# Kernel optimization log

Measured on AMD Instinct MI355X. Metric: run time of the kernel, lower is better.

The kernel has to match this reference:

```python
import jax, jax.numpy as jnp
import numpy as np

B, N, D, H = 4, 2048, 512, 8
DH = D // H
EPS = 1e-6


def setup_inputs() -> dict:
    key = jax.random.key(0)
    ks = jax.random.split(key, 12)
    s = 1.0 / np.sqrt(D)
    return {
        "x": jax.random.normal(ks[0], (B, N, D), jnp.float32),
        "attn_bias": jax.random.normal(ks[1], (B, 1, N, N), jnp.float32),
        "Wq": jax.random.normal(ks[2], (D, D), jnp.float32) * s,
        "bq": jnp.zeros((D,), jnp.float32),
        "Wk": jax.random.normal(ks[3], (D, D), jnp.float32) * s,
        "bk": jnp.zeros((D,), jnp.float32),
        "Wv": jax.random.normal(ks[4], (D, D), jnp.float32) * s,
        "bv": jnp.zeros((D,), jnp.float32),
        "Wo": jax.random.normal(ks[5], (D, D), jnp.float32) * s,
        "bo": jnp.zeros((D,), jnp.float32),
        "q_gamma": jnp.ones((DH,), jnp.float32),
        "q_beta": jnp.zeros((DH,), jnp.float32),
        "k_gamma": jnp.ones((DH,), jnp.float32),
        "k_beta": jnp.zeros((DH,), jnp.float32),
    }


def _layernorm(x, gamma, beta):
    mu = jnp.mean(x, axis=-1, keepdims=True)
    var = jnp.var(x, axis=-1, keepdims=True)
    return (x - mu) * jax.lax.rsqrt(var + EPS) * gamma + beta


def reference(x, attn_bias, Wq, bq, Wk, bk, Wv, bv, Wo, bo,
              q_gamma, q_beta, k_gamma, k_beta):
    b, n, d = x.shape
    # project and split heads: (B, H, N, DH)
    def heads(W, bias):
        return (x @ W.T + bias).reshape(b, n, H, DH).transpose(0, 2, 1, 3)
    q = heads(Wq, bq)
    k = heads(Wk, bk)
    v = heads(Wv, bv)
    q = _layernorm(q, q_gamma, q_beta)
    k = _layernorm(k, k_gamma, k_beta)
    scores = jnp.einsum('bhqd,bhkd->bhqk', q, k) / np.sqrt(DH)
    scores = scores + attn_bias  # (B,1,N,N) broadcasts over heads
    attn = jax.nn.softmax(scores, axis=-1)
    out = jnp.einsum('bhqk,bhkd->bhqd', attn, v)
    out = out.transpose(0, 2, 1, 3).reshape(b, n, d)
    return out @ Wo.T + bo
```

## Files before the change

kernel.cpp:

```cpp
#include <hip/hip_runtime.h>

typedef __attribute__((ext_vector_type(8))) short short8;
typedef __attribute__((ext_vector_type(4))) float f32x4;
typedef __attribute__((ext_vector_type(4))) int i32x4;
typedef __attribute__((ext_vector_type(4))) unsigned short u16x4;
typedef __attribute__((ext_vector_type(8))) unsigned short u16x8;
typedef __attribute__((ext_vector_type(2))) unsigned int u32x2;

#define B_  4
#define N_  2048
#define D_  512
#define H_  8
#define DH_ 64
#define M_  (B_ * N_)

__device__ __forceinline__ unsigned short f2bf(float f) {
    union { float f; unsigned u; } un; un.f = f;
    unsigned r = un.u + 0x7FFFu + ((un.u >> 16) & 1u);
    return (unsigned short)(r >> 16);
}
__device__ __forceinline__ float exp2fast(float x) {
#if __has_builtin(__builtin_amdgcn_exp2f)
    return __builtin_amdgcn_exp2f(x);
#else
    float r; asm("v_exp_f32 %0, %1" : "=v"(r) : "v"(x)); return r;
#endif
}
__device__ __forceinline__ unsigned cvtpk_bf16(float lo, float hi) {
    unsigned r;
    asm("v_cvt_pk_bf16_f32 %0, %1, %2" : "=v"(r) : "v"(lo), "v"(hi));
    return r;
}
__device__ __forceinline__ float max3f(float a, float b, float c) {
    return fmaxf(fmaxf(a, b), c);
}

typedef __attribute__((address_space(1))) const void gvoid;
typedef __attribute__((address_space(3))) void svoid;
__device__ __forceinline__ void load16_lds(const void* g, void* s) {
    __builtin_amdgcn_global_load_lds((gvoid*)g, (svoid*)s, 16, 0, 0);
}

__global__ __launch_bounds__(256) void cvt_all(
    const float* __restrict__ x,
    const float* __restrict__ W0, const float* __restrict__ W1,
    const float* __restrict__ W2, const float* __restrict__ W3,
    unsigned short* __restrict__ xb, unsigned short* __restrict__ Wb) {
    const int bx = blockIdx.x;
    const float* src;
    unsigned short* dst;
    int i;
    if (bx < 4096) {
        src = x; dst = xb;
        i = (bx * 256 + (int)threadIdx.x) * 4;
    } else {
        const int r = bx - 4096;
        const int sel = r >> 8;
        src = (sel == 0) ? W0 : (sel == 1) ? W1 : (sel == 2) ? W2 : W3;
        dst = Wb + (size_t)sel * D_ * D_;
        i = ((r & 255) * 256 + (int)threadIdx.x) * 4;
    }
    f32x4 v = *(const f32x4*)(src + i);
    u16x4 o;
    o[0] = f2bf(v[0]); o[1] = f2bf(v[1]); o[2] = f2bf(v[2]); o[3] = f2bf(v[3]);
    *(u16x4*)(dst + i) = o;
}

template <bool F32OUT, bool LNF>
__global__ __launch_bounds__(256, 2) void gemm_nt(
    const unsigned short* __restrict__ A,
    const unsigned short* __restrict__ W,
    const float* __restrict__ Bv0,
    const float* __restrict__ Bv1,
    const float* __restrict__ Bv2,
    const float* __restrict__ g0, const float* __restrict__ be0,
    const float* __restrict__ g1, const float* __restrict__ be1,
    unsigned short* __restrict__ outb,
    float* __restrict__ outf)
{
    const int mt = blockIdx.x;
    const int nt = blockIdx.y;
    const int sel = nt >> 2;
    const unsigned short* Wp = W + (size_t)sel * D_ * D_;
    const float* Bv = (sel == 0) ? Bv0 : (sel == 1) ? Bv1 : Bv2;
    const int n0 = (nt & 3) * 128;

    __shared__ __align__(16) unsigned short As[128 * 32];
    __shared__ __align__(16) unsigned short Bs[128 * 32];

    const int tid = threadIdx.x;
    const int w   = tid >> 6;
    const int l   = tid & 63;
    const int l15 = l & 15;
    const int qd  = l >> 4;
    const int wr  = w >> 1;
    const int wc  = w & 1;

    int srow[2], scol[2];
#pragma unroll
    for (int c = 0; c < 2; ++c) {
        const int g   = (w * 2 + c) * 64 + l;
        const int row = g >> 2;
        srow[c] = row;
        scol[c] = ((g & 3) ^ (row & 3)) * 8;
    }

    f32x4 acc[4][4];
#pragma unroll
    for (int i = 0; i < 4; ++i)
#pragma unroll
        for (int j = 0; j < 4; ++j)
            acc[i][j] = (f32x4){0.f, 0.f, 0.f, 0.f};

    const int swz = qd ^ (l15 & 3);

    for (int k0 = 0; k0 < D_; k0 += 32) {
        __syncthreads();
#pragma unroll
        for (int c = 0; c < 2; ++c) {
            load16_lds(A  + (size_t)(mt * 128 + srow[c]) * D_ + k0 + scol[c],
                       As + (w * 2 + c) * 512);
            load16_lds(Wp + (size_t)(n0 + srow[c]) * D_ + k0 + scol[c],
                       Bs + (w * 2 + c) * 512);
        }
        __syncthreads();

        short8 af[4], bfr[4];
#pragma unroll
        for (int rt = 0; rt < 4; ++rt)
            af[rt] = *(const short8*)&As[(wr * 64 + rt * 16 + l15) * 32 + swz * 8];
#pragma unroll
        for (int ct = 0; ct < 4; ++ct)
            bfr[ct] = *(const short8*)&Bs[(wc * 64 + ct * 16 + l15) * 32 + swz * 8];
#pragma unroll
        for (int rt = 0; rt < 4; ++rt)
#pragma unroll
            for (int ct = 0; ct < 4; ++ct)
                acc[rt][ct] = __builtin_amdgcn_mfma_f32_16x16x32_bf16(
                    af[rt], bfr[ct], acc[rt][ct], 0, 0, 0);
    }

    const float* gam = (sel == 0) ? g0 : g1;
    const float* bet = (sel == 0) ? be0 : be1;
    float gv[4], bv2[4];
    if (LNF) {
#pragma unroll
        for (int ct = 0; ct < 4; ++ct) { gv[ct] = gam[ct * 16 + l15]; bv2[ct] = bet[ct * 16 + l15]; }
    }

#pragma unroll
    for (int rt = 0; rt < 4; ++rt) {
        float v[4][4];
#pragma unroll
        for (int ct = 0; ct < 4; ++ct) {
            const float bias = Bv[n0 + wc * 64 + ct * 16 + l15];
#pragma unroll
            for (int r = 0; r < 4; ++r) v[ct][r] = acc[rt][ct][r] + bias;
        }
        if (LNF && sel < 2) {
#pragma unroll
            for (int r = 0; r < 4; ++r) {
                float s  = v[0][r] + v[1][r] + v[2][r] + v[3][r];
                float s2 = v[0][r]*v[0][r] + v[1][r]*v[1][r] + v[2][r]*v[2][r] + v[3][r]*v[3][r];
#pragma unroll
                for (int o = 1; o <= 8; o <<= 1) {
                    s  += __shfl_xor(s, o);
                    s2 += __shfl_xor(s2, o);
                }
                const float mu  = s * 0.015625f;
                const float var = s2 * 0.015625f - mu * mu;
                const float rs  = rsqrtf(var + 1e-6f);
#pragma unroll
                for (int ct = 0; ct < 4; ++ct)
                    v[ct][r] = (v[ct][r] - mu) * rs * gv[ct] + bv2[ct];
            }
        }
#pragma unroll
        for (int ct = 0; ct < 4; ++ct) {
            const int col  = n0 + wc * 64 + ct * 16 + l15;
            const int row0 = mt * 128 + wr * 64 + rt * 16 + qd * 4;
#pragma unroll
            for (int r = 0; r < 4; ++r) {
                const size_t oidx = (size_t)(row0 + r) * D_ + col;
                if (F32OUT) outf[oidx] = v[ct][r];
                else        outb[(size_t)sel * M_ * D_ + oidx] = f2bf(v[ct][r]);
            }
        }
    }
}

__global__ __launch_bounds__(256) void pack_kv(
    const unsigned short* __restrict__ K, const unsigned short* __restrict__ V,
    unsigned short* __restrict__ Kt, unsigned short* __restrict__ Vt2)
{
    const int nt = blockIdx.x, b = blockIdx.y;
    const int tid = threadIdx.x;
    __shared__ __align__(16) unsigned short Vl[64][520];

#pragma unroll
    for (int i = 0; i < 16; ++i) {
        const int c = i * 256 + tid;
        const int row = c >> 6, ch = c & 63;
        const size_t srow = ((size_t)(b * N_ + nt * 64 + row)) * D_ + ch * 8;
        i32x4 kd = *(const i32x4*)(K + srow);
        const int h = ch >> 3, dc = ch & 7;
        *(i32x4*)(Kt + ((((size_t)(b * 8 + h) * 32 + nt) * 64 + row) * 64) + dc * 8) = kd;
        i32x4 vd = *(const i32x4*)(V + srow);
        *(i32x4*)&Vl[row][ch * 8] = vd;
    }
    __syncthreads();
#pragma unroll
    for (int i = 0; i < 16; ++i) {
        const int c = i * 256 + tid;
        const int h = c >> 9, r = c & 511;
        const int dh = r >> 3, kc = r & 7;
        u16x4 o0, o1;
#pragma unroll
        for (int j = 0; j < 4; ++j) o0[j] = Vl[kc * 8 + j][h * 64 + dh];
#pragma unroll
        for (int j = 0; j < 4; ++j) o1[j] = Vl[kc * 8 + 4 + j][h * 64 + dh];
        const int t = kc >> 1;
        const int col0 = (t & 2) * 16 + (kc & 1) * 16 + (t & 1) * 4;
        const size_t rowbase = ((((size_t)(b * 8 + h) * 32 + nt) * 64 + dh) * 64);
        *(u16x4*)(Vt2 + rowbase + col0)     = o0;
        *(u16x4*)(Vt2 + rowbase + col0 + 8) = o1;
    }
}

__global__ __launch_bounds__(512, 4) void attn12(
    const unsigned short* __restrict__ Qm,
    const unsigned short* __restrict__ Kt,
    const unsigned short* __restrict__ Vt2,
    const float* __restrict__ Bias,
    unsigned short* __restrict__ AO)
{
    const int qt = blockIdx.x;
    const int h  = blockIdx.y;
    const int b  = blockIdx.z;
    const int w  = threadIdx.x >> 6;
    const int l  = threadIdx.x & 63;
    const int l15 = l & 15;
    const int qd  = l >> 4;
    const int q0 = qt * 128 + w * 16;
    const float L2E = 1.4426950408889634f;

    __shared__ __align__(16) unsigned char smem[32768];

    const int c    = w * 64 + l;
    const int srow = c >> 3;
    const int sg   = (c & 7) ^ (srow & 7);
    const int soff = srow * 64 + sg * 8;
    const int sc16 = c * 16;

    short8 qf[2];
#pragma unroll
    for (int hf = 0; hf < 2; ++hf)
        qf[hf] = *(const short8*)(Qm +
            (size_t)(b * N_ + q0 + l15) * D_ + h * DH_ + hf * 32 + qd * 8);

    f32x4 Ot[4];
#pragma unroll
    for (int rt = 0; rt < 4; ++rt) Ot[rt] = (f32x4){0.f, 0.f, 0.f, 0.f};
    float m_i = -3.0e38f;
    f32x4 li4 = (f32x4){0.f, 0.f, 0.f, 0.f};

    const unsigned short* Ktile0 = Kt  + (((size_t)(b * 8 + h) * 32) * 64) * 64;
    const unsigned short* Vtile0 = Vt2 + (((size_t)(b * 8 + h) * 32) * 64) * 64;
    const float* biasQ = Bias + ((size_t)b * N_ + q0 + l15) * N_;

    load16_lds(Ktile0 + soff, smem + sc16);
    load16_lds(Vtile0 + soff, smem + 8192 + sc16);
    f32x4 brA[4], brB[4];
#pragma unroll
    for (int rt = 0; rt < 4; ++rt)
        brA[rt] = *(const f32x4*)(biasQ + rt * 16 + qd * 4);
    asm volatile("s_waitcnt vmcnt(0)" ::: "memory");

#define ATTN_ITER(KT, CUR, BRC, BRN) do {                                      \
    unsigned char* Kbc = smem + (CUR) * 16384;                                 \
    unsigned char* Vbc = Kbc + 8192;                                           \
    asm volatile("s_waitcnt vmcnt(4)" ::: "memory");                           \
    __builtin_amdgcn_s_barrier();                                              \
    __builtin_amdgcn_sched_barrier(0);                                         \
    if ((KT) < 31) {                                                           \
        const unsigned short* Kn = Ktile0 + (size_t)((KT) + 1) * 4096;         \
        const unsigned short* Vn = Vtile0 + (size_t)((KT) + 1) * 4096;         \
        unsigned char* KbN = smem + (((CUR) ^ 1)) * 16384;                     \
        load16_lds(Kn + soff, KbN + sc16);                                     \
        load16_lds(Vn + soff, KbN + 8192 + sc16);                              \
    }                                                                          \
    asm volatile("" ::: "memory");       \
    {                                                                          \
        const float* Bn = biasQ + (size_t)(((KT) < 31) ? (KT) + 1 : 31) * 64;  \
        _Pragma("unroll")                                                      \
        for (int rt = 0; rt < 4; ++rt)                                         \
            BRN[rt] = *(const f32x4*)(Bn + rt * 16 + qd * 4);                  \
    }                                                                          \
    short8 kf[4][2];                                                           \
    _Pragma("unroll")                                                          \
    for (int rt = 0; rt < 4; ++rt) {                                           \
        const int kv = rt * 16 + l15;                                          \
        _Pragma("unroll")                                                      \
        for (int hf = 0; hf < 2; ++hf) {                                       \
            const int cidx = (hf * 4 + qd) ^ (kv & 7);                         \
            kf[rt][hf] = *(const short8*)(Kbc + kv * 128 + cidx * 16);         \
        }                                                                      \
    }                                                                          \
    f32x4 St[4];                                                               \
    __builtin_amdgcn_s_setprio(1);                                             \
    _Pragma("unroll")                                                          \
    for (int rt = 0; rt < 4; ++rt) {                                           \
        f32x4 v = (f32x4){0.f, 0.f, 0.f, 0.f};                                 \
        v = __builtin_amdgcn_mfma_f32_16x16x32_bf16(kf[rt][0], qf[0], v, 0, 0, 0); \
        v = __builtin_amdgcn_mfma_f32_16x16x32_bf16(kf[rt][1], qf[1], v, 0, 0, 0); \
        St[rt] = v;                                                            \
    }                                                                          \
    __builtin_amdgcn_s_setprio(0);                                             \
    short8 vf[4][2];                                                           \
    _Pragma("unroll")                                                          \
    for (int rt = 0; rt < 4; ++rt) {                                           \
        const int dh = rt * 16 + l15;                                          \
        _Pragma("unroll")                                                      \
        for (int hf = 0; hf < 2; ++hf) {                                       \
            const int cidx = (hf * 4 + qd) ^ (dh & 7);                         \
            vf[rt][hf] = *(const short8*)(Vbc + dh * 128 + cidx * 16);         \
        }                                                                      \
    }                                                                          \
    unsigned wq[4][2];                                                         \
    {                                                                          \
        f32x4 sv[4];                                                           \
        _Pragma("unroll")                                                      \
        for (int rt = 0; rt < 4; ++rt)                                         \
            sv[rt] = St[rt] * 0.125f + BRC[rt];                                \
        float mx0 = max3f(sv[0][0], sv[0][1], sv[0][2]);                       \
        float mx1 = max3f(sv[0][3], sv[1][0], sv[1][1]);                       \
        float mx2 = max3f(sv[1][2], sv[1][3], sv[2][0]);                       \
        float mx3 = max3f(sv[2][1], sv[2][2], sv[2][3]);                       \
        mx0 = max3f(mx0, sv[3][0], sv[3][1]);                                  \
        mx1 = max3f(mx1, sv[3][2], sv[3][3]);                                  \
        float mx = fmaxf(max3f(mx0, mx1, mx2), mx3);                           \
        mx = fmaxf(mx, __shfl_xor(mx, 16));                                    \
        mx = fmaxf(mx, __shfl_xor(mx, 32));                                    \
        if (__any(mx > m_i + 8.0f)) {                                          \
            const float mnew  = fmaxf(m_i, mx);                                \
            const float alpha = exp2fast((m_i - mnew) * L2E);                  \
            m_i = mnew;                                                        \
            li4 *= alpha;                                                      \
            _Pragma("unroll")                                                  \
            for (int rt = 0; rt < 4; ++rt) Ot[rt] *= alpha;                    \
        }                                                                      \
        const float mL = m_i * L2E;                                            \
        f32x4 p[4];                                                            \
        _Pragma("unroll")                                                      \
        for (int rt = 0; rt < 4; ++rt) {                                       \
            f32x4 e = sv[rt] * L2E - mL;                                       \
            p[rt][0] = exp2fast(e[0]); p[rt][1] = exp2fast(e[1]);              \
            p[rt][2] = exp2fast(e[2]); p[rt][3] = exp2fast(e[3]);              \
        }                                                                      \
        li4 += (p[0] + p[1]) + (p[2] + p[3]);                                  \
        _Pragma("unroll")                                                      \
        for (int rt = 0; rt < 4; ++rt) {                                       \
            wq[rt][0] = cvtpk_bf16(p[rt][0], p[rt][1]);                        \
            wq[rt][1] = cvtpk_bf16(p[rt][2], p[rt][3]);                        \
        }                                                                      \
    }                                                                          \
                           \
    union { unsigned u[4]; short8 s; } pk0, pk1;                               \
    pk0.u[0] = wq[0][0]; pk0.u[1] = wq[0][1];                                  \
    pk0.u[2] = wq[1][0]; pk0.u[3] = wq[1][1];                                  \
    pk1.u[0] = wq[2][0]; pk1.u[1] = wq[2][1];                                  \
    pk1.u[2] = wq[3][0]; pk1.u[3] = wq[3][1];                                  \
    __builtin_amdgcn_s_setprio(1);                                             \
    _Pragma("unroll")                                                          \
    for (int rt = 0; rt < 4; ++rt) {                                           \
        Ot[rt] = __builtin_amdgcn_mfma_f32_16x16x32_bf16(vf[rt][0], pk0.s, Ot[rt], 0, 0, 0); \
        Ot[rt] = __builtin_amdgcn_mfma_f32_16x16x32_bf16(vf[rt][1], pk1.s, Ot[rt], 0, 0, 0); \
    }                                                                          \
    __builtin_amdgcn_s_setprio(0);                                             \
} while (0)

    for (int kt2 = 0; kt2 < 16; ++kt2) {
        ATTN_ITER(kt2 * 2,     0, brA, brB);
        ATTN_ITER(kt2 * 2 + 1, 1, brB, brA);
    }
#undef ATTN_ITER

    float l_i = (li4[0] + li4[1]) + (li4[2] + li4[3]);
    l_i += __shfl_xor(l_i, 16);
    l_i += __shfl_xor(l_i, 32);
    const float inv = 1.f / l_i;
    const int q = q0 + l15;
#pragma unroll
    for (int rt = 0; rt < 4; ++rt) {
        u16x4 ob;
#pragma unroll
        for (int r = 0; r < 4; ++r) ob[r] = f2bf(Ot[rt][r] * inv);
        *(u16x4*)(AO + (size_t)(b * N_ + q) * D_ + h * DH_ + rt * 16 + qd * 4) = ob;
    }
}

extern "C" void kernel_launch(void* const* d_in, const int* in_sizes, int n_in,
                              void* d_out, int out_size, void* d_ws, size_t ws_size,
                              hipStream_t stream) {
    const float* x  = (const float*)d_in[0];
    const float* ab = (const float*)d_in[1];
    const float* Wq = (const float*)d_in[2];
    const float* bq = (const float*)d_in[3];
    const float* Wk = (const float*)d_in[4];
    const float* bk = (const float*)d_in[5];
    const float* Wv = (const float*)d_in[6];
    const float* bv = (const float*)d_in[7];
    const float* Wo = (const float*)d_in[8];
    const float* bo = (const float*)d_in[9];
    const float* qg = (const float*)d_in[10];
    const float* qb = (const float*)d_in[11];
    const float* kg = (const float*)d_in[12];
    const float* kb = (const float*)d_in[13];

    unsigned short* xb  = (unsigned short*)d_ws;
    unsigned short* Wb  = xb  + (size_t)M_ * D_;
    unsigned short* Y   = Wb  + (size_t)4 * D_ * D_;
    unsigned short* Kt  = Y   + (size_t)3 * M_ * D_;
    unsigned short* Vt2 = Kt  + (size_t)M_ * D_;
    unsigned short* AO  = Vt2 + (size_t)M_ * D_;
    float* out = (float*)d_out;

    cvt_all<<<dim3(5120), dim3(256), 0, stream>>>(x, Wq, Wk, Wv, Wo, xb, Wb);

    gemm_nt<false, true><<<dim3(64, 12), dim3(256), 0, stream>>>(
        xb, Wb, bq, bk, bv, qg, qb, kg, kb, Y, nullptr);

    pack_kv<<<dim3(32, 4), dim3(256), 0, stream>>>(
        Y + (size_t)M_ * D_, Y + (size_t)2 * M_ * D_, Kt, Vt2);

    attn12<<<dim3(16, 8, 4), dim3(512), 0, stream>>>(
        Y, Kt, Vt2, ab, AO);

    gemm_nt<true, false><<<dim3(64, 4), dim3(256), 0, stream>>>(
        AO, Wb + (size_t)3 * D_ * D_, bo, bo, bo,
        nullptr, nullptr, nullptr, nullptr, nullptr, out);
}
```

Measured before the change: 257.1 us.

## Give each attention wave two query tiles and read V directly from global

The attention kernel changes from 8 waves with 16 queries each to 4 waves with 32 queries each. Each K fragment loaded from LDS is now reused across two query tiles. V fragments are loaded straight from global memory in the pre-swizzled Vt2 layout rather than staged through LDS, so the LDS buffer halves and only K is double-buffered. Bias prefetch is no longer one tile ahead, and the wait is now vmcnt(0), which can expose global latency. Register pressure rises because accumulators and state are doubled.

```diff
diff --git a/kernel.cpp b/kernel.cpp
--- a/kernel.cpp
+++ b/kernel.cpp
@@ -4,7 +4,6 @@
 typedef __attribute__((ext_vector_type(4))) float f32x4;
 typedef __attribute__((ext_vector_type(4))) int i32x4;
 typedef __attribute__((ext_vector_type(4))) unsigned short u16x4;
-typedef __attribute__((ext_vector_type(8))) unsigned short u16x8;
 typedef __attribute__((ext_vector_type(2))) unsigned int u32x2;
 
 #define B_  4
@@ -227,7 +226,7 @@
     }
 }
 
-__global__ __launch_bounds__(512, 4) void attn12(
+__global__ __launch_bounds__(256, 2) void attn14(
     const unsigned short* __restrict__ Qm,
     const unsigned short* __restrict__ Kt,
     const unsigned short* __restrict__ Vt2,
@@ -241,61 +240,77 @@
     const int l  = threadIdx.x & 63;
     const int l15 = l & 15;
     const int qd  = l >> 4;
-    const int q0 = qt * 128 + w * 16;
+    const int q0 = qt * 128 + w * 32;
     const float L2E = 1.4426950408889634f;
 
-    __shared__ __align__(16) unsigned char smem[32768];
-
-    const int c    = w * 64 + l;
-    const int srow = c >> 3;
-    const int sg   = (c & 7) ^ (srow & 7);
-    const int soff = srow * 64 + sg * 8;
-    const int sc16 = c * 16;
-
-    short8 qf[2];
-#pragma unroll
-    for (int hf = 0; hf < 2; ++hf)
-        qf[hf] = *(const short8*)(Qm +
-            (size_t)(b * N_ + q0 + l15) * D_ + h * DH_ + hf * 32 + qd * 8);
-
-    f32x4 Ot[4];
-#pragma unroll
-    for (int rt = 0; rt < 4; ++rt) Ot[rt] = (f32x4){0.f, 0.f, 0.f, 0.f};
-    float m_i = -3.0e38f;
-    f32x4 li4 = (f32x4){0.f, 0.f, 0.f, 0.f};
+    __shared__ __align__(16) unsigned char smem[16384];
+
+    int soff[2], sc16[2];
+#pragma unroll
+    for (int i = 0; i < 2; ++i) {
+        const int c = (w * 2 + i) * 64 + l;
+        const int srow = c >> 3;
+        const int sg   = (c & 7) ^ (srow & 7);
+        soff[i] = srow * 64 + sg * 8;
+        sc16[i] = c * 16;
+    }
+
+    short8 qf[2][2];
+#pragma unroll
+    for (int ct = 0; ct < 2; ++ct)
+#pragma unroll
+        for (int hf = 0; hf < 2; ++hf)
+            qf[ct][hf] = *(const short8*)(Qm +
+                (size_t)(b * N_ + q0 + ct * 16 + l15) * D_ + h * DH_ + hf * 32 + qd * 8);
+
+    f32x4 Ot[4][2];
+#pragma unroll
+    for (int rt = 0; rt < 4; ++rt)
+#pragma unroll
+        for (int ct = 0; ct < 2; ++ct) Ot[rt][ct] = (f32x4){0.f, 0.f, 0.f, 0.f};
+    float m_i[2] = {-3.0e38f, -3.0e38f};
+    f32x4 li4[2];
+    li4[0] = (f32x4){0.f, 0.f, 0.f, 0.f};
+    li4[1] = (f32x4){0.f, 0.f, 0.f, 0.f};
 
     const unsigned short* Ktile0 = Kt  + (((size_t)(b * 8 + h) * 32) * 64) * 64;
     const unsigned short* Vtile0 = Vt2 + (((size_t)(b * 8 + h) * 32) * 64) * 64;
-    const float* biasQ = Bias + ((size_t)b * N_ + q0 + l15) * N_;
-
-    load16_lds(Ktile0 + soff, smem + sc16);
-    load16_lds(Vtile0 + soff, smem + 8192 + sc16);
-    f32x4 brA[4], brB[4];
-#pragma unroll
-    for (int rt = 0; rt < 4; ++rt)
-        brA[rt] = *(const f32x4*)(biasQ + rt * 16 + qd * 4);
-    asm volatile("s_waitcnt vmcnt(0)" ::: "memory");
-
-#define ATTN_ITER(KT, CUR, BRC, BRN) do {                                      \
-    unsigned char* Kbc = smem + (CUR) * 16384;                                 \
-    unsigned char* Vbc = Kbc + 8192;                                           \
-    asm volatile("s_waitcnt vmcnt(4)" ::: "memory");                           \
+    const float* bQ0 = Bias + ((size_t)b * N_ + q0 + l15) * N_;
+    const float* bQ1 = Bias + ((size_t)b * N_ + q0 + 16 + l15) * N_;
+
+    load16_lds(Ktile0 + soff[0], smem + sc16[0]);
+    load16_lds(Ktile0 + soff[1], smem + sc16[1]);
+
+#define ATTN_ITER(KT, CUR) do {                                                \
+    unsigned char* Kbc = smem + (CUR) * 8192;                                  \
+    asm volatile("s_waitcnt vmcnt(0)" ::: "memory");                           \
     __builtin_amdgcn_s_barrier();                                              \
     __builtin_amdgcn_sched_barrier(0);                                         \
+    f32x4 br[4][2];                                                            \
+    _Pragma("unroll")                                                          \
+    for (int rt = 0; rt < 4; ++rt) {                                           \
+        br[rt][0] = *(const f32x4*)(bQ0 + (size_t)(KT) * 64 + rt * 16 + qd * 4); \
+        br[rt][1] = *(const f32x4*)(bQ1 + (size_t)(KT) * 64 + rt * 16 + qd * 4); \
+    }                                                                          \
+    asm volatile("" ::: "memory");                    \
+    short8 vf[4][2];                                                           \
+    {                                                                          \
+        const unsigned short* Vtl = Vtile0 + (size_t)(KT) * 4096;              \
+        _Pragma("unroll")                                                      \
+        for (int rt = 0; rt < 4; ++rt)                                         \
+            _Pragma("unroll")                                                  \
+            for (int hf = 0; hf < 2; ++hf)                                     \
+                vf[rt][hf] = *(const short8*)(Vtl + (rt * 16 + l15) * 64 +     \
+                                              hf * 32 + qd * 8);               \
+    }                                                                          \
+    asm volatile("" ::: "memory");                     \
     if ((KT) < 31) {                                                           \
         const unsigned short* Kn = Ktile0 + (size_t)((KT) + 1) * 4096;         \
-        const unsigned short* Vn = Vtile0 + (size_t)((KT) + 1) * 4096;         \
-        unsigned char* KbN = smem + (((CUR) ^ 1)) * 16384;                     \
-        load16_lds(Kn + soff, KbN + sc16);                                     \
-        load16_lds(Vn + soff, KbN + 8192 + sc16);                              \
+        unsigned char* KbN = smem + (((CUR) ^ 1)) * 8192;                      \
+        load16_lds(Kn + soff[0], KbN + sc16[0]);                               \
+        load16_lds(Kn + soff[1], KbN + sc16[1]);                               \
     }                                                                          \
-    asm volatile("" ::: "memory");       \
-    {                                                                          \
-        const float* Bn = biasQ + (size_t)(((KT) < 31) ? (KT) + 1 : 31) * 64;  \
-        _Pragma("unroll")                                                      \
-        for (int rt = 0; rt < 4; ++rt)                                         \
-            BRN[rt] = *(const f32x4*)(Bn + rt * 16 + qd * 4);                  \
-    }                                                                          \
+    asm volatile("" ::: "memory");                                             \
     short8 kf[4][2];                                                           \
     _Pragma("unroll")                                                          \
     for (int rt = 0; rt < 4; ++rt) {                                           \
@@ -306,32 +321,24 @@
             kf[rt][hf] = *(const short8*)(Kbc + kv * 128 + cidx * 16);         \
         }                                                                      \
     }                                                                          \
-    f32x4 St[4];                                                               \
+    f32x4 St[4][2];                                                            \
     __builtin_amdgcn_s_setprio(1);                                             \
     _Pragma("unroll")                                                          \
-    for (int rt = 0; rt < 4; ++rt) {                                           \
-        f32x4 v = (f32x4){0.f, 0.f, 0.f, 0.f};                                 \
-        v = __builtin_amdgcn_mfma_f32_16x16x32_bf16(kf[rt][0], qf[0], v, 0, 0, 0); \
-        v = __builtin_amdgcn_mfma_f32_16x16x32_bf16(kf[rt][1], qf[1], v, 0, 0, 0); \
-        St[rt] = v;                                                            \
-    }                                                                          \
+    for (int rt = 0; rt < 4; ++rt)                                             \
+        _Pragma("unroll")                                                      \
+        for (int ct = 0; ct < 2; ++ct) {                                       \
+            f32x4 v = (f32x4){0.f, 0.f, 0.f, 0.f};                             \
+            v = __builtin_amdgcn_mfma_f32_16x16x32_bf16(kf[rt][0], qf[ct][0], v, 0, 0, 0); \
+            v = __builtin_amdgcn_mfma_f32_16x16x32_bf16(kf[rt][1], qf[ct][1], v, 0, 0, 0); \
+            St[rt][ct] = v;                                                    \
+        }                                                                      \
     __builtin_amdgcn_s_setprio(0);                                             \
-    short8 vf[4][2];                                                           \
     _Pragma("unroll")                                                          \
-    for (int rt = 0; rt < 4; ++rt) {                                           \
-        const int dh = rt * 16 + l15;                                          \
-        _Pragma("unroll")                                                      \
-        for (int hf = 0; hf < 2; ++hf) {                                       \
-            const int cidx = (hf * 4 + qd) ^ (dh & 7);                         \
-            vf[rt][hf] = *(const short8*)(Vbc + dh * 128 + cidx * 16);         \
-        }                                                                      \
-    }                                                                          \
-    unsigned wq[4][2];                                                         \
-    {                                                                          \
+    for (int ct = 0; ct < 2; ++ct) {                                           \
         f32x4 sv[4];                                                           \
         _Pragma("unroll")                                                      \
         for (int rt = 0; rt < 4; ++rt)                                         \
-            sv[rt] = St[rt] * 0.125f + BRC[rt];                                \
+            sv[rt] = St[rt][ct] * 0.125f + br[rt][ct];                         \
         float mx0 = max3f(sv[0][0], sv[0][1], sv[0][2]);                       \
         float mx1 = max3f(sv[0][3], sv[1][0], sv[1][1]);                       \
         float mx2 = max3f(sv[1][2], sv[1][3], sv[2][0]);                       \
@@ -341,15 +348,15 @@
         float mx = fmaxf(max3f(mx0, mx1, mx2), mx3);                           \
         mx = fmaxf(mx, __shfl_xor(mx, 16));                                    \
         mx = fmaxf(mx, __shfl_xor(mx, 32));                                    \
-        if (__any(mx > m_i + 8.0f)) {                                          \
-            const float mnew  = fmaxf(m_i, mx);                                \
-            const float alpha = exp2fast((m_i - mnew) * L2E);                  \
-            m_i = mnew;                                                        \
-            li4 *= alpha;                                                      \
+        if (__any(mx > m_i[ct] + 8.0f)) {                                      \
+            const float mnew  = fmaxf(m_i[ct], mx);                            \
+            const float alpha = exp2fast((m_i[ct] - mnew) * L2E);              \
+            m_i[ct] = mnew;                                                    \
+            li4[ct] *= alpha;                                                  \
             _Pragma("unroll")                                                  \
-            for (int rt = 0; rt < 4; ++rt) Ot[rt] *= alpha;                    \
+            for (int rt = 0; rt < 4; ++rt) Ot[rt][ct] *= alpha;                \
         }                                                                      \
-        const float mL = m_i * L2E;                                            \
+        const float mL = m_i[ct] * L2E;                                        \
         f32x4 p[4];                                                            \
         _Pragma("unroll")                                                      \
         for (int rt = 0; rt < 4; ++rt) {                                       \
@@ -357,45 +364,46 @@
             p[rt][0] = exp2fast(e[0]); p[rt][1] = exp2fast(e[1]);              \
             p[rt][2] = exp2fast(e[2]); p[rt][3] = exp2fast(e[3]);              \
         }                                                                      \
-        li4 += (p[0] + p[1]) + (p[2] + p[3]);                                  \
+        li4[ct] += (p[0] + p[1]) + (p[2] + p[3]);                              \
+        union { unsigned u[4]; short8 s; } pk0, pk1;                           \
+        pk0.u[0] = cvtpk_bf16(p[0][0], p[0][1]);                               \
+        pk0.u[1] = cvtpk_bf16(p[0][2], p[0][3]);                               \
+        pk0.u[2] = cvtpk_bf16(p[1][0], p[1][1]);                               \
+        pk0.u[3] = cvtpk_bf16(p[1][2], p[1][3]);                               \
+        pk1.u[0] = cvtpk_bf16(p[2][0], p[2][1]);                               \
+        pk1.u[1] = cvtpk_bf16(p[2][2], p[2][3]);                               \
+        pk1.u[2] = cvtpk_bf16(p[3][0], p[3][1]);                               \
+        pk1.u[3] = cvtpk_bf16(p[3][2], p[3][3]);                               \
+        __builtin_amdgcn_s_setprio(1);                                         \
         _Pragma("unroll")                                                      \
         for (int rt = 0; rt < 4; ++rt) {                                       \
-            wq[rt][0] = cvtpk_bf16(p[rt][0], p[rt][1]);                        \
-            wq[rt][1] = cvtpk_bf16(p[rt][2], p[rt][3]);                        \
+            Ot[rt][ct] = __builtin_amdgcn_mfma_f32_16x16x32_bf16(vf[rt][0], pk0.s, Ot[rt][ct], 0, 0, 0); \
+            Ot[rt][ct] = __builtin_amdgcn_mfma_f32_16x16x32_bf16(vf[rt][1], pk1.s, Ot[rt][ct], 0, 0, 0); \
         }                                                                      \
+        __builtin_amdgcn_s_setprio(0);                                         \
     }                                                                          \
-                           \
-    union { unsigned u[4]; short8 s; } pk0, pk1;                               \
-    pk0.u[0] = wq[0][0]; pk0.u[1] = wq[0][1];                                  \
-    pk0.u[2] = wq[1][0]; pk0.u[3] = wq[1][1];                                  \
-    pk1.u[0] = wq[2][0]; pk1.u[1] = wq[2][1];                                  \
-    pk1.u[2] = wq[3][0]; pk1.u[3] = wq[3][1];                                  \
-    __builtin_amdgcn_s_setprio(1);                                             \
-    _Pragma("unroll")                                                          \
-    for (int rt = 0; rt < 4; ++rt) {                                           \
-        Ot[rt] = __builtin_amdgcn_mfma_f32_16x16x32_bf16(vf[rt][0], pk0.s, Ot[rt], 0, 0, 0); \
-        Ot[rt] = __builtin_amdgcn_mfma_f32_16x16x32_bf16(vf[rt][1], pk1.s, Ot[rt], 0, 0, 0); \
-    }                                                                          \
-    __builtin_amdgcn_s_setprio(0);                                             \
 } while (0)
 
     for (int kt2 = 0; kt2 < 16; ++kt2) {
-        ATTN_ITER(kt2 * 2,     0, brA, brB);
-        ATTN_ITER(kt2 * 2 + 1, 1, brB, brA);
+        ATTN_ITER(kt2 * 2,     0);
+        ATTN_ITER(kt2 * 2 + 1, 1);
     }
 #undef ATTN_ITER
 
-    float l_i = (li4[0] + li4[1]) + (li4[2] + li4[3]);
-    l_i += __shfl_xor(l_i, 16);
-    l_i += __shfl_xor(l_i, 32);
-    const float inv = 1.f / l_i;
-    const int q = q0 + l15;
-#pragma unroll
-    for (int rt = 0; rt < 4; ++rt) {
-        u16x4 ob;
-#pragma unroll
-        for (int r = 0; r < 4; ++r) ob[r] = f2bf(Ot[rt][r] * inv);
-        *(u16x4*)(AO + (size_t)(b * N_ + q) * D_ + h * DH_ + rt * 16 + qd * 4) = ob;
+#pragma unroll
+    for (int ct = 0; ct < 2; ++ct) {
+        float l_i = (li4[ct][0] + li4[ct][1]) + (li4[ct][2] + li4[ct][3]);
+        l_i += __shfl_xor(l_i, 16);
+        l_i += __shfl_xor(l_i, 32);
+        const float inv = 1.f / l_i;
+        const int q = q0 + ct * 16 + l15;
+#pragma unroll
+        for (int rt = 0; rt < 4; ++rt) {
+            u16x4 ob;
+#pragma unroll
+            for (int r = 0; r < 4; ++r) ob[r] = f2bf(Ot[rt][ct][r] * inv);
+            *(u16x4*)(AO + (size_t)(b * N_ + q) * D_ + h * DH_ + rt * 16 + qd * 4) = ob;
+        }
     }
 }
 
@@ -433,7 +441,7 @@
     pack_kv<<<dim3(32, 4), dim3(256), 0, stream>>>(
         Y + (size_t)M_ * D_, Y + (size_t)2 * M_ * D_, Kt, Vt2);
 
-    attn12<<<dim3(16, 8, 4), dim3(512), 0, stream>>>(
+    attn14<<<dim3(16, 8, 4), dim3(256), 0, stream>>>(
         Y, Kt, Vt2, ab, AO);
 
     gemm_nt<true, false><<<dim3(64, 4), dim3(256), 0, stream>>>(
```

Result: slower. 294.0 us (+14.4%).
